# Optimization experiments

Measured on AMD Instinct MI355X. Metric: run time of the kernel, lower is better.

The kernel has to match this reference:

```python
import jax, jax.numpy as jnp
import numpy as np

B, L, D = 2, 2048, 1024
H, HD = 16, 64
MAX_LEN = 4096


def rotate_half(t):
    t1, t2 = jnp.split(t, 2, axis=-1)
    return jnp.concatenate([-t2, t1], axis=-1)


def setup_inputs() -> dict:
    key = jax.random.key(0)
    ks = jax.random.split(key, 6)
    # rope tables computed the standard way (cos/sin of position*inv_freq)
    inv_freq = 1.0 / (10000.0 ** (np.arange(0, HD, 2, dtype=np.float32) / HD))
    pos = np.arange(MAX_LEN, dtype=np.float32)
    freqs = np.einsum('l,f->lf', pos, inv_freq)          # [MAX_LEN, HD/2]
    emb = np.concatenate([freqs, freqs], axis=-1)        # [MAX_LEN, HD]
    return {
        'x': jax.random.normal(ks[0], (B, L, D), dtype=jnp.float32),
        'rope_cos': jnp.asarray(np.cos(emb)),
        'rope_sin': jnp.asarray(np.sin(emb)),
        'W_qkv': jax.random.normal(ks[1], (D, 3 * H * HD), dtype=jnp.float32) * (D ** -0.5),
        'W_out': jax.random.normal(ks[2], (H * HD, D), dtype=jnp.float32) * ((H * HD) ** -0.5),
        'b_out': jnp.zeros((D,), dtype=jnp.float32),
    }


def reference(x, rope_cos, rope_sin, W_qkv, W_out, b_out):
    Bb, Ll, Dd = x.shape
    qkv = jnp.einsum('bld,de->ble', x, W_qkv)            # fused QKV projection
    q, k, v = jnp.split(qkv, 3, axis=-1)
    # [B, h, L, d]
    q = q.reshape(Bb, Ll, H, HD).transpose(0, 2, 1, 3)
    k = k.reshape(Bb, Ll, H, HD).transpose(0, 2, 1, 3)
    v = v.reshape(Bb, Ll, H, HD).transpose(0, 2, 1, 3)
    cos = rope_cos[:Ll][None, None, :, :]                # [1,1,L,d]
    sin = rope_sin[:Ll][None, None, :, :]
    q = q * cos + rotate_half(q) * sin
    k = k * cos + rotate_half(k) * sin
    # causal scaled dot-product attention
    scale = HD ** -0.5
    scores = jnp.einsum('bhqd,bhkd->bhqk', q, k) * scale
    causal = jnp.tril(jnp.ones((Ll, Ll), dtype=bool))
    scores = jnp.where(causal[None, None], scores, jnp.finfo(scores.dtype).min)
    attn = jax.nn.softmax(scores, axis=-1)
    out = jnp.einsum('bhqk,bhkd->bhqd', attn, v)
    out = out.transpose(0, 2, 1, 3).reshape(Bb, Ll, H * HD)
    return jnp.einsum('ble,ed->bld', out, W_out) + b_out
```

## Files before the change

### kernel.cpp

```cpp
#include <hip/hip_runtime.h>
#include <math.h>

#define BQ 2
#define LQ 2048
#define DQ 1024
#define HQ 16
#define HDQ 64

typedef __bf16 bf16_t;
typedef bf16_t bf16x4 __attribute__((ext_vector_type(4)));
typedef bf16_t bf16x8 __attribute__((ext_vector_type(8)));
typedef float f32x4 __attribute__((ext_vector_type(4)));

__device__ __forceinline__ void gld16(const void* g, void* l) {
    __builtin_amdgcn_global_load_lds(
        (const __attribute__((address_space(1))) void*)g,
        (__attribute__((address_space(3))) void*)l, 16, 0, 0);
}

__global__ __launch_bounds__(256) void convert_kernel(
    const float* __restrict__ in, bf16_t* __restrict__ out)
{
    int i = (blockIdx.x * 256 + threadIdx.x) * 4;
    float4 v = *(const float4*)(in + i);
    bf16x4 o;
    o[0] = (bf16_t)v.x; o[1] = (bf16_t)v.y; o[2] = (bf16_t)v.z; o[3] = (bf16_t)v.w;
    *(bf16x4*)(out + i) = o;
}

__global__ __launch_bounds__(256) void transpose_bf16_kernel(
    const float* __restrict__ in, bf16_t* __restrict__ out, int K, int N)
{
    __shared__ float t[32][33];
    const int k0 = blockIdx.y * 32, n0 = blockIdx.x * 32;
    const int r = threadIdx.x >> 3, c4 = (threadIdx.x & 7) * 4;
    float4 v = *(const float4*)(in + (size_t)(k0 + r) * N + n0 + c4);
    t[r][c4 + 0] = v.x; t[r][c4 + 1] = v.y; t[r][c4 + 2] = v.z; t[r][c4 + 3] = v.w;
    __syncthreads();
    bf16x4 o;
    o[0] = (bf16_t)t[c4 + 0][r]; o[1] = (bf16_t)t[c4 + 1][r];
    o[2] = (bf16_t)t[c4 + 2][r]; o[3] = (bf16_t)t[c4 + 3][r];
    *(bf16x4*)(out + (size_t)(n0 + r) * K + k0 + c4) = o;
}

__global__ __launch_bounds__(256) void qkv_gemm_kernel(
    const bf16_t* __restrict__ A, const bf16_t* __restrict__ Bt,
    bf16_t* __restrict__ qo, bf16_t* __restrict__ ko, bf16_t* __restrict__ vo,
    const float* __restrict__ cosT, const float* __restrict__ sinT)
{
    __shared__ __align__(16) bf16_t As[128][64];
    __shared__ __align__(16) bf16_t Bs[128][64];
    const int K = 1024;
    const int tid  = threadIdx.x;
    const int lane = tid & 63;
    const int w    = tid >> 6;
    const int lr   = lane & 15, quad = lane >> 4;
    const int wm   = w & 1, wn = w >> 1;
    const int m0   = blockIdx.y * 128, n0 = blockIdx.x * 128;
    const int srow8 = lane >> 3;
    const int swz   = ((lane & 7) ^ srow8) * 8;

    f32x4 acc[4][4];
#pragma unroll
    for (int i = 0; i < 4; i++)
#pragma unroll
        for (int j = 0; j < 4; j++)
#pragma unroll
            for (int r = 0; r < 4; r++) acc[i][j][r] = 0.f;

    for (int k0 = 0; k0 < K; k0 += 64) {
        __syncthreads();
#pragma unroll
        for (int j = 0; j < 4; j++) {
            const int g = w * 4 + j;
            const int rr = g * 8 + srow8;
            gld16(A  + (size_t)(m0 + rr) * K + k0 + swz, &As[g * 8][0]);
            gld16(Bt + (size_t)(n0 + rr) * K + k0 + swz, &Bs[g * 8][0]);
        }
        __syncthreads();

        bf16x8 af[4][2], bfr[4][2];
#pragma unroll
        for (int t = 0; t < 4; t++)
#pragma unroll
            for (int h = 0; h < 2; h++) {
                const int cA = ((quad + 4 * h) ^ (lr & 7)) * 8;
                af[t][h]  = *(const bf16x8*)(&As[wm * 64 + t * 16 + lr][cA]);
                bfr[t][h] = *(const bf16x8*)(&Bs[wn * 64 + t * 16 + lr][cA]);
            }
#pragma unroll
        for (int h = 0; h < 2; h++)
#pragma unroll
            for (int mt = 0; mt < 4; mt++)
#pragma unroll
                for (int nt = 0; nt < 4; nt++)
                    acc[mt][nt] = __builtin_amdgcn_mfma_f32_16x16x32_bf16(
                        af[mt][h], bfr[nt][h], acc[mt][nt], 0, 0, 0);
    }

    const int which = n0 >> 10;
    const int h = ((n0 & 1023) + wn * 64) >> 6;
    if (which == 2) {
#pragma unroll
        for (int mt = 0; mt < 4; mt++) {
            const int m = m0 + wm * 64 + mt * 16 + quad * 4;
            const int b = m >> 11, l = m & 2047;
            bf16_t* p = vo + ((size_t)(b * HQ + h) * HDQ) * LQ + l;
#pragma unroll
            for (int nt = 0; nt < 4; nt++) {
                bf16x4 pv;
#pragma unroll
                for (int r = 0; r < 4; r++) pv[r] = (bf16_t)acc[mt][nt][r];
                *(bf16x4*)(p + (size_t)(nt * 16 + lr) * LQ) = pv;
            }
        }
    } else {
        bf16_t* dst = which ? ko : qo;
        const float qs = which ? 1.0f : 0.18033688011f;
#pragma unroll
        for (int mt = 0; mt < 4; mt++)
#pragma unroll
            for (int r = 0; r < 4; r++) {
                const int m = m0 + wm * 64 + mt * 16 + quad * 4 + r;
                const int b = m >> 11, l = m & 2047;
                const float c0 = cosT[l * 64 + lr];
                const float c1 = cosT[l * 64 + 16 + lr];
                const float s0 = sinT[l * 64 + lr];
                const float s1 = sinT[l * 64 + 16 + lr];
                const float a0 = acc[mt][0][r], a1 = acc[mt][1][r];
                const float a2 = acc[mt][2][r], a3 = acc[mt][3][r];
                bf16_t* p = dst + ((size_t)(b * HQ + h) * LQ + l) * HDQ;
                p[lr]      = (bf16_t)((a0 * c0 - a2 * s0) * qs);
                p[16 + lr] = (bf16_t)((a1 * c1 - a3 * s1) * qs);
                p[32 + lr] = (bf16_t)((a2 * c0 + a0 * s0) * qs);
                p[48 + lr] = (bf16_t)((a3 * c1 + a1 * s1) * qs);
            }
    }
}

__global__ __launch_bounds__(256) void out_gemm_kernel(
    const bf16_t* __restrict__ A, const bf16_t* __restrict__ Bt,
    float* __restrict__ fo, const float* __restrict__ bias)
{
    __shared__ __align__(16) bf16_t As[64][64];
    __shared__ __align__(16) bf16_t Bs[128][64];
    const int K = 1024, N = 1024;
    const int tid  = threadIdx.x;
    const int lane = tid & 63;
    const int w    = tid >> 6;
    const int lr   = lane & 15, quad = lane >> 4;
    const int m0   = blockIdx.y * 64, n0 = blockIdx.x * 128;
    const int srow8 = lane >> 3;
    const int swz   = ((lane & 7) ^ srow8) * 8;

    f32x4 acc[4][2];
#pragma unroll
    for (int i = 0; i < 4; i++)
#pragma unroll
        for (int j = 0; j < 2; j++)
#pragma unroll
            for (int r = 0; r < 4; r++) acc[i][j][r] = 0.f;

    for (int k0 = 0; k0 < K; k0 += 64) {
        __syncthreads();
#pragma unroll
        for (int j = 0; j < 2; j++) {
            const int g = w * 2 + j;
            gld16(A + (size_t)(m0 + g * 8 + srow8) * K + k0 + swz, &As[g * 8][0]);
        }
#pragma unroll
        for (int j = 0; j < 4; j++) {
            const int g = w * 4 + j;
            gld16(Bt + (size_t)(n0 + g * 8 + srow8) * K + k0 + swz, &Bs[g * 8][0]);
        }
        __syncthreads();

        bf16x8 af[4][2], bfr[2][2];
#pragma unroll
        for (int h = 0; h < 2; h++) {
            const int cA = ((quad + 4 * h) ^ (lr & 7)) * 8;
#pragma unroll
            for (int t = 0; t < 4; t++)
                af[t][h] = *(const bf16x8*)(&As[t * 16 + lr][cA]);
#pragma unroll
            for (int t = 0; t < 2; t++)
                bfr[t][h] = *(const bf16x8*)(&Bs[w * 32 + t * 16 + lr][cA]);
        }
#pragma unroll
        for (int h = 0; h < 2; h++)
#pragma unroll
            for (int mt = 0; mt < 4; mt++)
#pragma unroll
                for (int nt = 0; nt < 2; nt++)
                    acc[mt][nt] = __builtin_amdgcn_mfma_f32_16x16x32_bf16(
                        af[mt][h], bfr[nt][h], acc[mt][nt], 0, 0, 0);
    }

#pragma unroll
    for (int nt = 0; nt < 2; nt++) {
        const int n = n0 + w * 32 + nt * 16 + lr;
        const float bj = bias[n];
#pragma unroll
        for (int mt = 0; mt < 4; mt++)
#pragma unroll
            for (int r = 0; r < 4; r++) {
                const int m = m0 + mt * 16 + quad * 4 + r;
                fo[(size_t)m * N + n] = acc[mt][nt][r] + bj;
            }
    }
}

__global__ __launch_bounds__(256) void attn_kernel5(
    const bf16_t* __restrict__ qb, const bf16_t* __restrict__ kb,
    const bf16_t* __restrict__ vtb, bf16_t* __restrict__ ob)
{
    __shared__ __align__(16) bf16_t Kb[2][64][80];
    __shared__ __align__(16) bf16_t Vs[2][64][80];
    __shared__ __align__(16) bf16_t Pb[4][16][72];

    const int tid  = threadIdx.x;
    const int lane = tid & 63;
    const int w    = tid >> 6;
    const int quad = lane >> 4;
    const int lr   = lane & 15;
    const int bh   = blockIdx.x;
    const int qt   = 31 - blockIdx.y;

    const bf16_t* Kh = kb  + (size_t)bh * LQ * HDQ;
    const bf16_t* Vh = vtb + (size_t)bh * HDQ * LQ;

    const int r0 = tid >> 3, c0 = (tid & 7) * 8;
    const int r1 = r0 + 32;

    bf16x8 ones;
#pragma unroll
    for (int j = 0; j < 8; j++) ones[j] = (bf16_t)1.0f;

    const int qrow = qt * 64 + w * 16 + lr;
    const bf16_t* qp = qb + ((size_t)bh * LQ + qrow) * HDQ;
    const bf16x8 qa0 = *(const bf16x8*)(qp + quad * 8);
    const bf16x8 qa1 = *(const bf16x8*)(qp + 32 + quad * 8);

    bf16x8 kp0 = *(const bf16x8*)(Kh + (size_t)r0 * HDQ + c0);
    bf16x8 kp1 = *(const bf16x8*)(Kh + (size_t)r1 * HDQ + c0);
    bf16x8 vp0 = *(const bf16x8*)(Vh + (size_t)r0 * LQ + c0);
    bf16x8 vp1 = *(const bf16x8*)(Vh + (size_t)r1 * LQ + c0);

    f32x4 Oacc[4], lacc;
#pragma unroll
    for (int nt = 0; nt < 4; nt++)
#pragma unroll
        for (int r = 0; r < 4; r++) Oacc[nt][r] = 0.f;
#pragma unroll
    for (int r = 0; r < 4; r++) lacc[r] = 0.f;

    for (int kt = 0; kt <= qt; kt++) {
        const int buf = kt & 1;
        *(bf16x8*)(&Kb[buf][r0][c0]) = kp0;
        *(bf16x8*)(&Kb[buf][r1][c0]) = kp1;
        *(bf16x8*)(&Vs[buf][r0][c0]) = vp0;
        *(bf16x8*)(&Vs[buf][r1][c0]) = vp1;
        __syncthreads();
        if (kt < qt) {
            const bf16_t* kn = Kh + (size_t)(kt + 1) * 64 * HDQ;
            kp0 = *(const bf16x8*)(kn + (size_t)r0 * HDQ + c0);
            kp1 = *(const bf16x8*)(kn + (size_t)r1 * HDQ + c0);
            vp0 = *(const bf16x8*)(Vh + (size_t)r0 * LQ + (kt + 1) * 64 + c0);
            vp1 = *(const bf16x8*)(Vh + (size_t)r1 * LQ + (kt + 1) * 64 + c0);
        }

        f32x4 s[4];
#pragma unroll
        for (int nt = 0; nt < 4; nt++) {
            const bf16x8 kf0 = *(const bf16x8*)(&Kb[buf][nt * 16 + lr][quad * 8]);
            const bf16x8 kf1 = *(const bf16x8*)(&Kb[buf][nt * 16 + lr][32 + quad * 8]);
            f32x4 z = {0.f, 0.f, 0.f, 0.f};
            z = __builtin_amdgcn_mfma_f32_16x16x32_bf16(qa0, kf0, z, 0, 0, 0);
            z = __builtin_amdgcn_mfma_f32_16x16x32_bf16(qa1, kf1, z, 0, 0, 0);
            s[nt] = z;
        }
        if (kt == qt) {
#pragma unroll
            for (int nt = 0; nt < 4; nt++)
#pragma unroll
                for (int r = 0; r < 4; r++)
                    if (nt * 16 + lr > w * 16 + quad * 4 + r) s[nt][r] = -INFINITY;
        }
#pragma unroll
        for (int nt = 0; nt < 4; nt++)
#pragma unroll
            for (int r = 0; r < 4; r++)
                s[nt][r] = __builtin_amdgcn_exp2f(s[nt][r]);
#pragma unroll
        for (int nt = 0; nt < 4; nt++)
#pragma unroll
            for (int r = 0; r < 4; r++)
                Pb[w][quad * 4 + r][nt * 16 + lr] = (bf16_t)s[nt][r];
        const bf16x8 pa0 = *(const bf16x8*)(&Pb[w][lr][quad * 8]);
        const bf16x8 pa1 = *(const bf16x8*)(&Pb[w][lr][32 + quad * 8]);

#pragma unroll
        for (int nt = 0; nt < 4; nt++) {
            const bf16x8 vf0 = *(const bf16x8*)(&Vs[buf][nt * 16 + lr][quad * 8]);
            const bf16x8 vf1 = *(const bf16x8*)(&Vs[buf][nt * 16 + lr][32 + quad * 8]);
            Oacc[nt] = __builtin_amdgcn_mfma_f32_16x16x32_bf16(pa0, vf0, Oacc[nt], 0, 0, 0);
            Oacc[nt] = __builtin_amdgcn_mfma_f32_16x16x32_bf16(pa1, vf1, Oacc[nt], 0, 0, 0);
        }
        lacc = __builtin_amdgcn_mfma_f32_16x16x32_bf16(pa0, ones, lacc, 0, 0, 0);
        lacc = __builtin_amdgcn_mfma_f32_16x16x32_bf16(pa1, ones, lacc, 0, 0, 0);
    }

    const int b = bh >> 4, h = bh & 15;
#pragma unroll
    for (int r = 0; r < 4; r++) {
        const float inv = 1.0f / lacc[r];
        const int q = qt * 64 + w * 16 + quad * 4 + r;
        bf16_t* op = ob + ((size_t)(b * LQ + q)) * 1024 + h * 64;
#pragma unroll
        for (int nt = 0; nt < 4; nt++)
            op[nt * 16 + lr] = (bf16_t)(Oacc[nt][r] * inv);
    }
}

extern "C" void kernel_launch(void* const* d_in, const int* in_sizes, int n_in,
                              void* d_out, int out_size, void* d_ws, size_t ws_size,
                              hipStream_t stream) {
    const float* x        = (const float*)d_in[0];
    const float* rope_cos = (const float*)d_in[1];
    const float* rope_sin = (const float*)d_in[2];
    const float* W_qkv    = (const float*)d_in[3];
    const float* W_out    = (const float*)d_in[4];
    const float* b_out    = (const float*)d_in[5];
    float* out = (float*)d_out;

    char* wsb = (char*)d_ws;
    bf16_t* xb    = (bf16_t*)(wsb);
    bf16_t* qbf   = (bf16_t*)(wsb + ((size_t)8  << 20));
    bf16_t* kbf   = (bf16_t*)(wsb + ((size_t)16 << 20));
    bf16_t* vtb   = (bf16_t*)(wsb + ((size_t)24 << 20));
    bf16_t* ob    = (bf16_t*)(wsb + ((size_t)32 << 20));
    bf16_t* Wqkvt = (bf16_t*)(wsb + ((size_t)40 << 20));
    bf16_t* Wot   = (bf16_t*)(wsb + ((size_t)46 << 20));

    convert_kernel<<<(4096 * 1024 / 4) / 256, 256, 0, stream>>>(x, xb);
    dim3 gt1(3072 / 32, 1024 / 32);
    transpose_bf16_kernel<<<gt1, 256, 0, stream>>>(W_qkv, Wqkvt, 1024, 3072);
    dim3 gt2(1024 / 32, 1024 / 32);
    transpose_bf16_kernel<<<gt2, 256, 0, stream>>>(W_out, Wot, 1024, 1024);

    dim3 g1(3072 / 128, 4096 / 128);
    qkv_gemm_kernel<<<g1, 256, 0, stream>>>(xb, Wqkvt, qbf, kbf, vtb,
                                            rope_cos, rope_sin);

    dim3 g2(32, 32);
    attn_kernel5<<<g2, 256, 0, stream>>>(qbf, kbf, vtb, ob);

    dim3 g3(1024 / 128, 4096 / 64);
    out_gemm_kernel<<<g3, 256, 0, stream>>>(ob, Wot, out, b_out);
}
```

Baseline: 183.7 us.

## Keep softmax P in registers via transposed S and f16 PV MFMA; merge prep kernels

The attention kernel now computes S transposed (K as the A operand), so each lane's exp'd scores already match the f16 16x16x16 MFMA A-operand layout. This removes the per-tile LDS round trip for P, and V is stored as f16 to match. Separately, the three prep launches are merged into one kernel that also packs the rope cos/sin values into float4 so the QKV epilogue does one vector load instead of four scalar loads. This trades bf16 for f16 precision on P and V and uses twice as many smaller MFMAs for PV.

```diff
diff --git a/kernel.cpp b/kernel.cpp
--- a/kernel.cpp
+++ b/kernel.cpp
@@ -10,6 +10,9 @@
 typedef __bf16 bf16_t;
 typedef bf16_t bf16x4 __attribute__((ext_vector_type(4)));
 typedef bf16_t bf16x8 __attribute__((ext_vector_type(8)));
+typedef _Float16 f16_t;
+typedef f16_t f16x4 __attribute__((ext_vector_type(4)));
+typedef f16_t f16x8 __attribute__((ext_vector_type(8)));
 typedef float f32x4 __attribute__((ext_vector_type(4)));
 
 __device__ __forceinline__ void gld16(const void* g, void* l) {
@@ -18,35 +21,50 @@
         (__attribute__((address_space(3))) void*)l, 16, 0, 0);
 }
 
-__global__ __launch_bounds__(256) void convert_kernel(
-    const float* __restrict__ in, bf16_t* __restrict__ out)
-{
-    int i = (blockIdx.x * 256 + threadIdx.x) * 4;
-    float4 v = *(const float4*)(in + i);
-    bf16x4 o;
-    o[0] = (bf16_t)v.x; o[1] = (bf16_t)v.y; o[2] = (bf16_t)v.z; o[3] = (bf16_t)v.w;
-    *(bf16x4*)(out + i) = o;
-}
-
-__global__ __launch_bounds__(256) void transpose_bf16_kernel(
-    const float* __restrict__ in, bf16_t* __restrict__ out, int K, int N)
+__global__ __launch_bounds__(256) void prep_kernel(
+    const float* __restrict__ x, const float* __restrict__ Wqkv,
+    const float* __restrict__ Wout, const float* __restrict__ cosT,
+    const float* __restrict__ sinT,
+    bf16_t* __restrict__ xb, bf16_t* __restrict__ Wqkvt,
+    bf16_t* __restrict__ Wot, float4* __restrict__ rpk)
 {
     __shared__ float t[32][33];
-    const int k0 = blockIdx.y * 32, n0 = blockIdx.x * 32;
-    const int r = threadIdx.x >> 3, c4 = (threadIdx.x & 7) * 4;
-    float4 v = *(const float4*)(in + (size_t)(k0 + r) * N + n0 + c4);
-    t[r][c4 + 0] = v.x; t[r][c4 + 1] = v.y; t[r][c4 + 2] = v.z; t[r][c4 + 3] = v.w;
-    __syncthreads();
-    bf16x4 o;
-    o[0] = (bf16_t)t[c4 + 0][r]; o[1] = (bf16_t)t[c4 + 1][r];
-    o[2] = (bf16_t)t[c4 + 2][r]; o[3] = (bf16_t)t[c4 + 3][r];
-    *(bf16x4*)(out + (size_t)(n0 + r) * K + k0 + c4) = o;
+    const int bid = blockIdx.x, tid = threadIdx.x;
+    if (bid < 4096) {
+        const int i = (bid * 256 + tid) * 4;
+        float4 v = *(const float4*)(x + i);
+        bf16x4 o;
+        o[0] = (bf16_t)v.x; o[1] = (bf16_t)v.y; o[2] = (bf16_t)v.z; o[3] = (bf16_t)v.w;
+        *(bf16x4*)(xb + i) = o;
+    } else if (bid < 8192) {
+        const bool isq = bid < 7168;
+        const int b = isq ? bid - 4096 : bid - 7168;
+        const int N = isq ? 3072 : 1024;
+        const int gx = isq ? 96 : 32;
+        const float* in = isq ? Wqkv : Wout;
+        bf16_t* out = isq ? Wqkvt : Wot;
+        const int k0 = (b / gx) * 32, n0 = (b % gx) * 32;
+        const int r = tid >> 3, c4 = (tid & 7) * 4;
+        float4 v = *(const float4*)(in + (size_t)(k0 + r) * N + n0 + c4);
+        t[r][c4 + 0] = v.x; t[r][c4 + 1] = v.y;
+        t[r][c4 + 2] = v.z; t[r][c4 + 3] = v.w;
+        __syncthreads();
+        bf16x4 o;
+        o[0] = (bf16_t)t[c4 + 0][r]; o[1] = (bf16_t)t[c4 + 1][r];
+        o[2] = (bf16_t)t[c4 + 2][r]; o[3] = (bf16_t)t[c4 + 3][r];
+        *(bf16x4*)(out + (size_t)(n0 + r) * 1024 + k0 + c4) = o;
+    } else {
+        const int idx = (bid - 8192) * 256 + tid;
+        const int i = idx & 15, l = idx >> 4;
+        rpk[idx] = make_float4(cosT[l * 64 + i], cosT[l * 64 + 16 + i],
+                               sinT[l * 64 + i], sinT[l * 64 + 16 + i]);
+    }
 }
 
 __global__ __launch_bounds__(256) void qkv_gemm_kernel(
     const bf16_t* __restrict__ A, const bf16_t* __restrict__ Bt,
-    bf16_t* __restrict__ qo, bf16_t* __restrict__ ko, bf16_t* __restrict__ vo,
-    const float* __restrict__ cosT, const float* __restrict__ sinT)
+    bf16_t* __restrict__ qo, bf16_t* __restrict__ ko, f16_t* __restrict__ vo,
+    const float4* __restrict__ rpk)
 {
     __shared__ __align__(16) bf16_t As[128][64];
     __shared__ __align__(16) bf16_t Bs[128][64];
@@ -105,13 +123,13 @@
         for (int mt = 0; mt < 4; mt++) {
             const int m = m0 + wm * 64 + mt * 16 + quad * 4;
             const int b = m >> 11, l = m & 2047;
-            bf16_t* p = vo + ((size_t)(b * HQ + h) * HDQ) * LQ + l;
+            f16_t* p = vo + ((size_t)(b * HQ + h) * HDQ) * LQ + l;
 #pragma unroll
             for (int nt = 0; nt < 4; nt++) {
-                bf16x4 pv;
-#pragma unroll
-                for (int r = 0; r < 4; r++) pv[r] = (bf16_t)acc[mt][nt][r];
-                *(bf16x4*)(p + (size_t)(nt * 16 + lr) * LQ) = pv;
+                f16x4 pv;
+#pragma unroll
+                for (int r = 0; r < 4; r++) pv[r] = (f16_t)acc[mt][nt][r];
+                *(f16x4*)(p + (size_t)(nt * 16 + lr) * LQ) = pv;
             }
         }
     } else {
@@ -123,17 +141,14 @@
             for (int r = 0; r < 4; r++) {
                 const int m = m0 + wm * 64 + mt * 16 + quad * 4 + r;
                 const int b = m >> 11, l = m & 2047;
-                const float c0 = cosT[l * 64 + lr];
-                const float c1 = cosT[l * 64 + 16 + lr];
-                const float s0 = sinT[l * 64 + lr];
-                const float s1 = sinT[l * 64 + 16 + lr];
+                const float4 rp = rpk[l * 16 + lr];
                 const float a0 = acc[mt][0][r], a1 = acc[mt][1][r];
                 const float a2 = acc[mt][2][r], a3 = acc[mt][3][r];
                 bf16_t* p = dst + ((size_t)(b * HQ + h) * LQ + l) * HDQ;
-                p[lr]      = (bf16_t)((a0 * c0 - a2 * s0) * qs);
-                p[16 + lr] = (bf16_t)((a1 * c1 - a3 * s1) * qs);
-                p[32 + lr] = (bf16_t)((a2 * c0 + a0 * s0) * qs);
-                p[48 + lr] = (bf16_t)((a3 * c1 + a1 * s1) * qs);
+                p[lr]      = (bf16_t)((a0 * rp.x - a2 * rp.z) * qs);
+                p[16 + lr] = (bf16_t)((a1 * rp.y - a3 * rp.w) * qs);
+                p[32 + lr] = (bf16_t)((a2 * rp.x + a0 * rp.z) * qs);
+                p[48 + lr] = (bf16_t)((a3 * rp.y + a1 * rp.w) * qs);
             }
     }
 }
@@ -210,13 +225,12 @@
     }
 }
 
-__global__ __launch_bounds__(256) void attn_kernel5(
+__global__ __launch_bounds__(256) void attn_kernel6(
     const bf16_t* __restrict__ qb, const bf16_t* __restrict__ kb,
-    const bf16_t* __restrict__ vtb, bf16_t* __restrict__ ob)
+    const f16_t* __restrict__ vtb, bf16_t* __restrict__ ob)
 {
     __shared__ __align__(16) bf16_t Kb[2][64][80];
-    __shared__ __align__(16) bf16_t Vs[2][64][80];
-    __shared__ __align__(16) bf16_t Pb[4][16][72];
+    __shared__ __align__(16) f16_t  Vs[2][64][72];
 
     const int tid  = threadIdx.x;
     const int lane = tid & 63;
@@ -227,14 +241,14 @@
     const int qt   = 31 - blockIdx.y;
 
     const bf16_t* Kh = kb  + (size_t)bh * LQ * HDQ;
-    const bf16_t* Vh = vtb + (size_t)bh * HDQ * LQ;
+    const f16_t*  Vh = vtb + (size_t)bh * HDQ * LQ;
 
     const int r0 = tid >> 3, c0 = (tid & 7) * 8;
     const int r1 = r0 + 32;
 
-    bf16x8 ones;
-#pragma unroll
-    for (int j = 0; j < 8; j++) ones[j] = (bf16_t)1.0f;
+    f16x4 ones;
+#pragma unroll
+    for (int j = 0; j < 4; j++) ones[j] = (f16_t)1.0f;
 
     const int qrow = qt * 64 + w * 16 + lr;
     const bf16_t* qp = qb + ((size_t)bh * LQ + qrow) * HDQ;
@@ -243,14 +257,14 @@
 
     bf16x8 kp0 = *(const bf16x8*)(Kh + (size_t)r0 * HDQ + c0);
     bf16x8 kp1 = *(const bf16x8*)(Kh + (size_t)r1 * HDQ + c0);
-    bf16x8 vp0 = *(const bf16x8*)(Vh + (size_t)r0 * LQ + c0);
-    bf16x8 vp1 = *(const bf16x8*)(Vh + (size_t)r1 * LQ + c0);
+    f16x8  vp0 = *(const f16x8*)(Vh + (size_t)r0 * LQ + c0);
+    f16x8  vp1 = *(const f16x8*)(Vh + (size_t)r1 * LQ + c0);
 
     f32x4 Oacc[4], lacc;
 #pragma unroll
-    for (int nt = 0; nt < 4; nt++)
-#pragma unroll
-        for (int r = 0; r < 4; r++) Oacc[nt][r] = 0.f;
+    for (int d = 0; d < 4; d++)
+#pragma unroll
+        for (int r = 0; r < 4; r++) Oacc[d][r] = 0.f;
 #pragma unroll
     for (int r = 0; r < 4; r++) lacc[r] = 0.f;
 
@@ -258,15 +272,15 @@
         const int buf = kt & 1;
         *(bf16x8*)(&Kb[buf][r0][c0]) = kp0;
         *(bf16x8*)(&Kb[buf][r1][c0]) = kp1;
-        *(bf16x8*)(&Vs[buf][r0][c0]) = vp0;
-        *(bf16x8*)(&Vs[buf][r1][c0]) = vp1;
+        *(f16x8*)(&Vs[buf][r0][c0]) = vp0;
+        *(f16x8*)(&Vs[buf][r1][c0]) = vp1;
         __syncthreads();
         if (kt < qt) {
             const bf16_t* kn = Kh + (size_t)(kt + 1) * 64 * HDQ;
             kp0 = *(const bf16x8*)(kn + (size_t)r0 * HDQ + c0);
             kp1 = *(const bf16x8*)(kn + (size_t)r1 * HDQ + c0);
-            vp0 = *(const bf16x8*)(Vh + (size_t)r0 * LQ + (kt + 1) * 64 + c0);
-            vp1 = *(const bf16x8*)(Vh + (size_t)r1 * LQ + (kt + 1) * 64 + c0);
+            vp0 = *(const f16x8*)(Vh + (size_t)r0 * LQ + (kt + 1) * 64 + c0);
+            vp1 = *(const f16x8*)(Vh + (size_t)r1 * LQ + (kt + 1) * 64 + c0);
         }
 
         f32x4 s[4];
@@ -275,8 +289,8 @@
             const bf16x8 kf0 = *(const bf16x8*)(&Kb[buf][nt * 16 + lr][quad * 8]);
             const bf16x8 kf1 = *(const bf16x8*)(&Kb[buf][nt * 16 + lr][32 + quad * 8]);
             f32x4 z = {0.f, 0.f, 0.f, 0.f};
-            z = __builtin_amdgcn_mfma_f32_16x16x32_bf16(qa0, kf0, z, 0, 0, 0);
-            z = __builtin_amdgcn_mfma_f32_16x16x32_bf16(qa1, kf1, z, 0, 0, 0);
+            z = __builtin_amdgcn_mfma_f32_16x16x32_bf16(kf0, qa0, z, 0, 0, 0);
+            z = __builtin_amdgcn_mfma_f32_16x16x32_bf16(kf1, qa1, z, 0, 0, 0);
             s[nt] = z;
         }
         if (kt == qt) {
@@ -284,30 +298,25 @@
             for (int nt = 0; nt < 4; nt++)
 #pragma unroll
                 for (int r = 0; r < 4; r++)
-                    if (nt * 16 + lr > w * 16 + quad * 4 + r) s[nt][r] = -INFINITY;
-        }
+                    if (nt * 16 + quad * 4 + r > w * 16 + lr) s[nt][r] = -INFINITY;
+        }
+        f16x4 pa[4];
 #pragma unroll
         for (int nt = 0; nt < 4; nt++)
 #pragma unroll
             for (int r = 0; r < 4; r++)
-                s[nt][r] = __builtin_amdgcn_exp2f(s[nt][r]);
+                pa[nt][r] = (f16_t)__builtin_amdgcn_exp2f(s[nt][r]);
+
+#pragma unroll
+        for (int d = 0; d < 4; d++)
+#pragma unroll
+            for (int nt = 0; nt < 4; nt++) {
+                const f16x4 vf = *(const f16x4*)(&Vs[buf][d * 16 + lr][nt * 16 + quad * 4]);
+                Oacc[d] = __builtin_amdgcn_mfma_f32_16x16x16f16(pa[nt], vf, Oacc[d], 0, 0, 0);
+            }
 #pragma unroll
         for (int nt = 0; nt < 4; nt++)
-#pragma unroll
-            for (int r = 0; r < 4; r++)
-                Pb[w][quad * 4 + r][nt * 16 + lr] = (bf16_t)s[nt][r];
-        const bf16x8 pa0 = *(const bf16x8*)(&Pb[w][lr][quad * 8]);
-        const bf16x8 pa1 = *(const bf16x8*)(&Pb[w][lr][32 + quad * 8]);
-
-#pragma unroll
-        for (int nt = 0; nt < 4; nt++) {
-            const bf16x8 vf0 = *(const bf16x8*)(&Vs[buf][nt * 16 + lr][quad * 8]);
-            const bf16x8 vf1 = *(const bf16x8*)(&Vs[buf][nt * 16 + lr][32 + quad * 8]);
-            Oacc[nt] = __builtin_amdgcn_mfma_f32_16x16x32_bf16(pa0, vf0, Oacc[nt], 0, 0, 0);
-            Oacc[nt] = __builtin_amdgcn_mfma_f32_16x16x32_bf16(pa1, vf1, Oacc[nt], 0, 0, 0);
-        }
-        lacc = __builtin_amdgcn_mfma_f32_16x16x32_bf16(pa0, ones, lacc, 0, 0, 0);
-        lacc = __builtin_amdgcn_mfma_f32_16x16x32_bf16(pa1, ones, lacc, 0, 0, 0);
+            lacc = __builtin_amdgcn_mfma_f32_16x16x16f16(pa[nt], ones, lacc, 0, 0, 0);
     }
 
     const int b = bh >> 4, h = bh & 15;
@@ -317,8 +326,8 @@
         const int q = qt * 64 + w * 16 + quad * 4 + r;
         bf16_t* op = ob + ((size_t)(b * LQ + q)) * 1024 + h * 64;
 #pragma unroll
-        for (int nt = 0; nt < 4; nt++)
-            op[nt * 16 + lr] = (bf16_t)(Oacc[nt][r] * inv);
+        for (int d = 0; d < 4; d++)
+            op[d * 16 + lr] = (bf16_t)(Oacc[d][r] * inv);
     }
 }
 
@@ -337,23 +346,20 @@
     bf16_t* xb    = (bf16_t*)(wsb);
     bf16_t* qbf   = (bf16_t*)(wsb + ((size_t)8  << 20));
     bf16_t* kbf   = (bf16_t*)(wsb + ((size_t)16 << 20));
-    bf16_t* vtb   = (bf16_t*)(wsb + ((size_t)24 << 20));
+    f16_t*  vth   = (f16_t*) (wsb + ((size_t)24 << 20));
     bf16_t* ob    = (bf16_t*)(wsb + ((size_t)32 << 20));
     bf16_t* Wqkvt = (bf16_t*)(wsb + ((size_t)40 << 20));
     bf16_t* Wot   = (bf16_t*)(wsb + ((size_t)46 << 20));
-
-    convert_kernel<<<(4096 * 1024 / 4) / 256, 256, 0, stream>>>(x, xb);
-    dim3 gt1(3072 / 32, 1024 / 32);
-    transpose_bf16_kernel<<<gt1, 256, 0, stream>>>(W_qkv, Wqkvt, 1024, 3072);
-    dim3 gt2(1024 / 32, 1024 / 32);
-    transpose_bf16_kernel<<<gt2, 256, 0, stream>>>(W_out, Wot, 1024, 1024);
+    float4* rpk   = (float4*)(wsb + ((size_t)48 << 20));
+
+    prep_kernel<<<8320, 256, 0, stream>>>(x, W_qkv, W_out, rope_cos, rope_sin,
+                                          xb, Wqkvt, Wot, rpk);
 
     dim3 g1(3072 / 128, 4096 / 128);
-    qkv_gemm_kernel<<<g1, 256, 0, stream>>>(xb, Wqkvt, qbf, kbf, vtb,
-                                            rope_cos, rope_sin);
+    qkv_gemm_kernel<<<g1, 256, 0, stream>>>(xb, Wqkvt, qbf, kbf, vth, rpk);
 
     dim3 g2(32, 32);
-    attn_kernel5<<<g2, 256, 0, stream>>>(qbf, kbf, vtb, ob);
+    attn_kernel6<<<g2, 256, 0, stream>>>(qbf, kbf, vth, ob);
 
     dim3 g3(1024 / 128, 4096 / 64);
     out_gemm_kernel<<<g3, 256, 0, stream>>>(ob, Wot, out, b_out);
```

Result: no change. 184.1 us (+0.2%).
